# Kernel optimization log

Hardware: AMD Instinct MI355X
Metric: run time of the kernel (lower is better)

## Reference

```python
import jax, jax.numpy as jnp
import numpy as np
import math

DIM = 512


def setup_inputs() -> dict:
    key = jax.random.key(0)
    ks = jax.random.split(key, 6)
    B, N, D = 4, 4096, DIM
    H = D // 2
    features = jax.random.normal(ks[0], (B, N, D), dtype=jnp.float32)
    W1 = jax.random.normal(ks[1], (D, H), dtype=jnp.float32) * 0.02
    b1 = jnp.zeros((H,), dtype=jnp.float32)
    ln_g = jnp.ones((H,), dtype=jnp.float32)
    ln_b = jnp.zeros((H,), dtype=jnp.float32)
    W2 = jax.random.normal(ks[2], (H, 1), dtype=jnp.float32) * 0.02
    b2 = jnp.zeros((1,), dtype=jnp.float32)
    target_entropy = jnp.ones((1,), dtype=jnp.float32) * math.log(D)
    temperature = jnp.ones((1,), dtype=jnp.float32)
    return {"features": features, "W1": W1, "b1": b1, "ln_g": ln_g,
            "ln_b": ln_b, "W2": W2, "b2": b2,
            "target_entropy": target_entropy, "temperature": temperature}


def _layernorm(x, g, b, eps=1e-5):
    mu = jnp.mean(x, axis=-1, keepdims=True)
    var = jnp.mean((x - mu) ** 2, axis=-1, keepdims=True)
    return (x - mu) * jax.lax.rsqrt(var + eps) * g + b


def reference(features, W1, b1, ln_g, ln_b, W2, b2, target_entropy, temperature):
    # ---- compute_entropy: pairwise RBF kernel over [B, N, D] ----
    sq = jnp.sum(features ** 2, axis=-1)                       # [B, N]
    gram = jnp.einsum('bnd,bmd->bnm', features, features)      # [B, N, N]
    d2 = jnp.maximum(sq[:, :, None] + sq[:, None, :] - 2.0 * gram, 0.0)
    tau = temperature[0]
    kernel = jnp.exp(-d2 / (2.0 * tau ** 2))                   # [B, N, N]
    probs = kernel / jnp.sum(kernel, axis=-1, keepdims=True)
    entropy = -jnp.sum(probs * jnp.log(probs + 1e-6), axis=-1)  # [B, N]

    # ---- entropy estimator MLP (computed in original forward, output unused) ----
    h = features @ W1 + b1
    h = _layernorm(h, ln_g, ln_b)
    h = jax.nn.gelu(h, approximate=False)
    estimated_entropy = h @ W2 + b2                            # [B, N, 1] (unused)
    del estimated_entropy

    # ---- sigmoid-gated control signal ----
    entropy_diff = entropy - target_entropy[0]
    control_signal = jax.nn.sigmoid(-entropy_diff / tau)       # [B, N]
    controlled_features = features * control_signal[..., None]
    return controlled_features, control_signal
```

## Files before the change

### kernel.cpp

```cpp
#include <hip/hip_runtime.h>
#include <stdint.h>

#define N_TOK 4096
#define DIM   512
#define BATCH 4
#define BN    (BATCH * N_TOK)
#define JSPLIT 8
#define IPW   64
#define IPB   256
#define NG    (N_TOK / JSPLIT / 16)

typedef __attribute__((ext_vector_type(4))) float f32x4;
typedef __attribute__((ext_vector_type(8))) int   i32x8;

typedef const __attribute__((address_space(1))) uint32_t* gptr_t;
typedef __attribute__((address_space(3))) uint32_t* lptr_t;

__device__ __forceinline__ float sumsq8(uint lo, uint hi) {
    float s = 0.f, f;
    f = __builtin_amdgcn_cvt_f32_fp8((int)lo, 0); s = fmaf(f, f, s);
    f = __builtin_amdgcn_cvt_f32_fp8((int)lo, 1); s = fmaf(f, f, s);
    f = __builtin_amdgcn_cvt_f32_fp8((int)lo, 2); s = fmaf(f, f, s);
    f = __builtin_amdgcn_cvt_f32_fp8((int)lo, 3); s = fmaf(f, f, s);
    f = __builtin_amdgcn_cvt_f32_fp8((int)hi, 0); s = fmaf(f, f, s);
    f = __builtin_amdgcn_cvt_f32_fp8((int)hi, 1); s = fmaf(f, f, s);
    f = __builtin_amdgcn_cvt_f32_fp8((int)hi, 2); s = fmaf(f, f, s);
    f = __builtin_amdgcn_cvt_f32_fp8((int)hi, 3); s = fmaf(f, f, s);
    return s;
}

__global__ __launch_bounds__(256) void prep_kernel(
    const float* __restrict__ feat, uint8_t* __restrict__ fb,
    uint8_t* __restrict__ fbT, float* __restrict__ sq)
{
    __shared__ __align__(16) long lt[1024];
    const int t = threadIdx.x;
    const int row16 = t >> 4, seg = t & 15;
    const size_t grp = blockIdx.x;
    const size_t row = grp * 16 + row16;

    const float4* src = (const float4*)(feat + row * DIM + seg * 32);
    uint32_t wd[8];
    float s = 0.f;
#pragma unroll
    for (int i = 0; i < 4; ++i) {
        float4 a = src[2 * i], b = src[2 * i + 1];
        uint lo = (uint)__builtin_amdgcn_cvt_pk_fp8_f32(a.x, a.y, 0, false);
        lo      = (uint)__builtin_amdgcn_cvt_pk_fp8_f32(a.z, a.w, (int)lo, true);
        uint hi = (uint)__builtin_amdgcn_cvt_pk_fp8_f32(b.x, b.y, 0, false);
        hi      = (uint)__builtin_amdgcn_cvt_pk_fp8_f32(b.z, b.w, (int)hi, true);
        wd[2 * i] = lo; wd[2 * i + 1] = hi;
        s += sumsq8(lo, hi);
    }

    uint4* dst = (uint4*)(fb + row * DIM + seg * 32);
    uint4 o0; o0.x = wd[0]; o0.y = wd[1]; o0.z = wd[2]; o0.w = wd[3];
    uint4 o1; o1.x = wd[4]; o1.y = wd[5]; o1.z = wd[6]; o1.w = wd[7];
    dst[0] = o0; dst[1] = o1;

#pragma unroll
    for (int i = 0; i < 4; ++i) {
        int c = seg * 4 + i;
        long d = ((long)(unsigned)wd[2 * i + 1] << 32) | (unsigned)wd[2 * i];
        lt[c * 16 + ((row16 + c) & 15)] = d;
    }

#pragma unroll
    for (int m = 1; m < 16; m <<= 1) s += __shfl_xor(s, m);
    if (seg == 0) sq[row] = s;

    __syncthreads();
    long* ot = (long*)(fbT + grp * 8192);
#pragma unroll
    for (int i = 0; i < 4; ++i) {
        int p    = t + i * 256;
        int kk   = p >> 8;
        int rem  = p & 255;
        int half = rem >> 7;
        int l6   = (rem >> 1) & 63;
        int qq   = l6 >> 4;
        int r    = l6 & 15;
        int w8   = half * 2 + (p & 1);
        int c    = kk * 16 + qq * 4 + w8;
        ot[p] = lt[c * 16 + ((r + c) & 15)];
    }
}

__global__ __launch_bounds__(256, 2) void entropy_kernel(
    const uint8_t* __restrict__ fb, const uint8_t* __restrict__ fbT,
    const float* __restrict__ sq, const float* __restrict__ temp,
    float* __restrict__ Sp, float* __restrict__ Tp)
{
    __shared__ uint4 Bs[4][512];
    __shared__ float sqlds[NG * 16];
    const int t    = threadIdx.x;
    const int w    = t >> 6;
    const int lane = t & 63;
    const int q    = lane >> 4;
    const int c16  = lane & 15;
    const int lbo  = lane * 16;

    const int flat  = blockIdx.x;
    const int combo = flat & 31;
    const int batch = combo >> 3;
    const int jh    = combo & 7;
    const int iblk  = flat >> 5;
    const int iw    = iblk * IPB + w * IPW;
    const size_t rowbase = (size_t)batch * N_TOK;

    const float tau    = temp[0];
    const float inv2t2 = 0.5f / (tau * tau);
    const float cg     = 1.0f / (tau * tau);

    i32x8 afrag[4][4];
#pragma unroll
    for (int s = 0; s < 4; ++s) {
        const uint4* ap = (const uint4*)(fb + (rowbase + iw + s * 16 + c16) * DIM);
#pragma unroll
        for (int kk = 0; kk < 4; ++kk) {
            uint4 lo = ap[kk * 8 + q * 2];
            uint4 hi = ap[kk * 8 + q * 2 + 1];
            i32x8 v = {(int)lo.x, (int)lo.y, (int)lo.z, (int)lo.w,
                       (int)hi.x, (int)hi.y, (int)hi.z, (int)hi.w};
            afrag[s][kk] = v;
        }
    }
    float pi[4][4];
#pragma unroll
    for (int s = 0; s < 4; ++s)
#pragma unroll
        for (int r = 0; r < 4; ++r)
            pi[s][r] = -sq[rowbase + iw + s * 16 + q * 4 + r] * inv2t2;

    {
        const float* sqslice = sq + rowbase + (size_t)jh * (N_TOK / JSPLIT);
        sqlds[t]       = sqslice[t];
        sqlds[t + 256] = sqslice[t + 256];
    }

    float S[4][4], T[4][4];
#pragma unroll
    for (int s = 0; s < 4; ++s)
#pragma unroll
        for (int r = 0; r < 4; ++r) { S[s][r] = 0.f; T[s][r] = 0.f; }

    const uint8_t* bgbase = fbT
        + ((size_t)batch * (N_TOK / 16) + (size_t)jh * NG) * 8192;

    auto stage = [&](int g) {
        const uint8_t* gs = bgbase + (size_t)g * 8192 + w * 2048 + lbo;
        uint8_t* ld = (uint8_t*)(&Bs[g & 3][0]) + w * 2048;
        __builtin_amdgcn_global_load_lds((gptr_t)(const void*)gs,
                                         (lptr_t)(void*)ld, 16, 0, 0);
        __builtin_amdgcn_global_load_lds((gptr_t)(const void*)(gs + 1024),
                                         (lptr_t)(void*)(ld + 1024), 16, 0, 0);
    };
    stage(0);
    stage(1);
    asm volatile("s_waitcnt lgkmcnt(0)" ::: "memory");

    for (int g = 0; g < NG; ++g) {
        if (g + 2 < NG) stage(g + 2);
        if (g + 2 < NG)      asm volatile("s_waitcnt vmcnt(4)" ::: "memory");
        else if (g + 1 < NG) asm volatile("s_waitcnt vmcnt(2)" ::: "memory");
        else                 asm volatile("s_waitcnt vmcnt(0)" ::: "memory");
        __builtin_amdgcn_s_barrier();
        __builtin_amdgcn_sched_barrier(0);

        const uint8_t* bs = (const uint8_t*)(&Bs[g & 3][0]);
        float pj = -sqlds[g * 16 + c16] * inv2t2;
        f32x4 acc[4] = {{0,0,0,0},{0,0,0,0},{0,0,0,0},{0,0,0,0}};
        __builtin_amdgcn_s_setprio(1);
#pragma unroll
        for (int kk = 0; kk < 4; ++kk) {
            uint4 lo = *(const uint4*)(bs + kk * 2048 + lbo);
            uint4 hi = *(const uint4*)(bs + kk * 2048 + 1024 + lbo);
            i32x8 b = {(int)lo.x, (int)lo.y, (int)lo.z, (int)lo.w,
                       (int)hi.x, (int)hi.y, (int)hi.z, (int)hi.w};
            acc[0] = __builtin_amdgcn_mfma_scale_f32_16x16x128_f8f6f4(afrag[0][kk], b, acc[0], 0, 0, 0, 127, 0, 127);
            acc[1] = __builtin_amdgcn_mfma_scale_f32_16x16x128_f8f6f4(afrag[1][kk], b, acc[1], 0, 0, 0, 127, 0, 127);
            acc[2] = __builtin_amdgcn_mfma_scale_f32_16x16x128_f8f6f4(afrag[2][kk], b, acc[2], 0, 0, 0, 127, 0, 127);
            acc[3] = __builtin_amdgcn_mfma_scale_f32_16x16x128_f8f6f4(afrag[3][kk], b, acc[3], 0, 0, 0, 127, 0, 127);
        }
        __builtin_amdgcn_s_setprio(0);
        float m = -1e30f;
#pragma unroll
        for (int s = 0; s < 4; ++s)
#pragma unroll
            for (int r = 0; r < 4; ++r) {
                acc[s][r] = fmaf(acc[s][r], cg, pi[s][r] + pj);
                m = fmaxf(m, acc[s][r]);
            }
        if (m > -110.0f) {
#pragma unroll
            for (int s = 0; s < 4; ++s)
#pragma unroll
                for (int r = 0; r < 4; ++r) {
                    float ee = fminf(acc[s][r], 0.f);
                    float k  = __expf(ee);
                    S[s][r] += k;
                    T[s][r]  = fmaf(k, ee, T[s][r]);
                }
        }
    }

#pragma unroll
    for (int m = 1; m < 16; m <<= 1)
#pragma unroll
        for (int s = 0; s < 4; ++s)
#pragma unroll
            for (int r = 0; r < 4; ++r) {
                S[s][r] += __shfl_xor(S[s][r], m);
                T[s][r] += __shfl_xor(T[s][r], m);
            }

    if (c16 == 0) {
#pragma unroll
        for (int s = 0; s < 4; ++s)
#pragma unroll
            for (int r = 0; r < 4; ++r) {
                size_t idx = (size_t)jh * BN + rowbase + iw + s * 16 + q * 4 + r;
                Sp[idx] = S[s][r];
                Tp[idx] = T[s][r];
            }
    }
}

__global__ __launch_bounds__(256) void finalize_kernel(
    const float* __restrict__ feat, const float* __restrict__ Sp,
    const float* __restrict__ Tp, const float* __restrict__ tgt,
    const float* __restrict__ temp, float* __restrict__ out)
{
    int row  = (blockIdx.x << 2) + (threadIdx.x >> 6);
    int lane = threadIdx.x & 63;
    float S = 0.0f, T = 0.0f;
#pragma unroll
    for (int j = 0; j < JSPLIT; ++j) {
        S += Sp[(size_t)j * BN + row];
        T += Tp[(size_t)j * BN + row];
    }
    float tau = temp[0];
    float E  = __logf(S) - T / S;
    float cs = 1.0f / (1.0f + __expf((E - tgt[0]) / tau));

    const float4* F4 = (const float4*)(feat + (size_t)row * DIM);
    float4*       O4 = (float4*)(out + (size_t)row * DIM);
    float4 v0 = F4[lane], v1 = F4[lane + 64];
    v0.x *= cs; v0.y *= cs; v0.z *= cs; v0.w *= cs;
    v1.x *= cs; v1.y *= cs; v1.z *= cs; v1.w *= cs;
    O4[lane] = v0; O4[lane + 64] = v1;
    if (lane == 0) out[(size_t)BN * DIM + row] = cs;
}

extern "C" void kernel_launch(void* const* d_in, const int* in_sizes, int n_in,
                              void* d_out, int out_size, void* d_ws, size_t ws_size,
                              hipStream_t stream) {
    const float* feat = (const float*)d_in[0];
    const float* tgt  = (const float*)d_in[7];
    const float* temp = (const float*)d_in[8];
    float* out = (float*)d_out;

    char* ws = (char*)d_ws;
    uint8_t* fb  = (uint8_t*)ws;
    uint8_t* fbT = fb + (size_t)BN * DIM;
    float*   sq  = (float*)(fbT + (size_t)BN * DIM);
    float*   Sp  = sq + BN;
    float*   Tp  = Sp + (size_t)JSPLIT * BN;

    prep_kernel<<<dim3(BN / 16), dim3(256), 0, stream>>>(feat, fb, fbT, sq);
    entropy_kernel<<<dim3((N_TOK / IPB) * BATCH * JSPLIT), dim3(256), 0, stream>>>(fb, fbT, sq, temp, Sp, Tp);
    finalize_kernel<<<dim3(BN / 4), dim3(256), 0, stream>>>(feat, Sp, Tp, tgt, temp, out);
}
```

Baseline: 148.4 us.

## Use per-wave private LDS ring, drop row-major fp8 copy, bound-based exp skip

Each wave now stages the full B tile into its own double-buffered LDS slot. This removes the block-wide s_barrier from the inner loop; the next stage is issued after the MFMA reads complete. The row-major fp8 buffer is dropped and A fragments are loaded from the transposed fbT layout, which cuts prep writes. The skip test now uses an upper bound from the raw accumulator max and the max row norm, so the per-element FMA only runs when needed. Each wave now loads 4x more B data from global/L2 because tiles are no longer shared across the four waves, and LDS use doubles.

```diff
diff --git a/kernel.cpp b/kernel.cpp
--- a/kernel.cpp
+++ b/kernel.cpp
@@ -30,8 +30,8 @@
 }
 
 __global__ __launch_bounds__(256) void prep_kernel(
-    const float* __restrict__ feat, uint8_t* __restrict__ fb,
-    uint8_t* __restrict__ fbT, float* __restrict__ sq)
+    const float* __restrict__ feat, uint8_t* __restrict__ fbT,
+    float* __restrict__ sq)
 {
     __shared__ __align__(16) long lt[1024];
     const int t = threadIdx.x;
@@ -52,11 +52,6 @@
         wd[2 * i] = lo; wd[2 * i + 1] = hi;
         s += sumsq8(lo, hi);
     }
-
-    uint4* dst = (uint4*)(fb + row * DIM + seg * 32);
-    uint4 o0; o0.x = wd[0]; o0.y = wd[1]; o0.z = wd[2]; o0.w = wd[3];
-    uint4 o1; o1.x = wd[4]; o1.y = wd[5]; o1.z = wd[6]; o1.w = wd[7];
-    dst[0] = o0; dst[1] = o1;
 
 #pragma unroll
     for (int i = 0; i < 4; ++i) {
@@ -87,11 +82,11 @@
 }
 
 __global__ __launch_bounds__(256, 2) void entropy_kernel(
-    const uint8_t* __restrict__ fb, const uint8_t* __restrict__ fbT,
+    const uint8_t* __restrict__ fbT,
     const float* __restrict__ sq, const float* __restrict__ temp,
     float* __restrict__ Sp, float* __restrict__ Tp)
 {
-    __shared__ uint4 Bs[4][512];
+    __shared__ uint4 ring[4][2][512];
     __shared__ float sqlds[NG * 16];
     const int t    = threadIdx.x;
     const int w    = t >> 6;
@@ -110,28 +105,31 @@
 
     const float tau    = temp[0];
     const float inv2t2 = 0.5f / (tau * tau);
-    const float cg     = 1.0f / (tau * tau);
+    const float cg_    = 1.0f / (tau * tau);
 
     i32x8 afrag[4][4];
 #pragma unroll
     for (int s = 0; s < 4; ++s) {
-        const uint4* ap = (const uint4*)(fb + (rowbase + iw + s * 16 + c16) * DIM);
+        const uint8_t* ga = fbT + ((rowbase + iw) / 16 + s) * 8192;
 #pragma unroll
         for (int kk = 0; kk < 4; ++kk) {
-            uint4 lo = ap[kk * 8 + q * 2];
-            uint4 hi = ap[kk * 8 + q * 2 + 1];
+            uint4 lo = *(const uint4*)(ga + kk * 2048 + lbo);
+            uint4 hi = *(const uint4*)(ga + kk * 2048 + 1024 + lbo);
             i32x8 v = {(int)lo.x, (int)lo.y, (int)lo.z, (int)lo.w,
                        (int)hi.x, (int)hi.y, (int)hi.z, (int)hi.w};
             afrag[s][kk] = v;
         }
     }
-    float pi[4][4];
-#pragma unroll
-    for (int s = 0; s < 4; ++s)
-#pragma unroll
-        for (int r = 0; r < 4; ++r)
-            pi[s][r] = -sq[rowbase + iw + s * 16 + q * 4 + r] * inv2t2;
-
+    float pi_[4][4];
+    float pim = -1e30f;
+#pragma unroll
+    for (int s = 0; s < 4; ++s) {
+        float4 p4 = *(const float4*)(sq + rowbase + iw + s * 16 + q * 4);
+        pi_[s][0] = -p4.x * inv2t2; pi_[s][1] = -p4.y * inv2t2;
+        pi_[s][2] = -p4.z * inv2t2; pi_[s][3] = -p4.w * inv2t2;
+        pim = fmaxf(pim, fmaxf(fmaxf(pi_[s][0], pi_[s][1]),
+                               fmaxf(pi_[s][2], pi_[s][3])));
+    }
     {
         const float* sqslice = sq + rowbase + (size_t)jh * (N_TOK / JSPLIT);
         sqlds[t]       = sqslice[t];
@@ -147,56 +145,68 @@
     const uint8_t* bgbase = fbT
         + ((size_t)batch * (N_TOK / 16) + (size_t)jh * NG) * 8192;
 
-    auto stage = [&](int g) {
-        const uint8_t* gs = bgbase + (size_t)g * 8192 + w * 2048 + lbo;
-        uint8_t* ld = (uint8_t*)(&Bs[g & 3][0]) + w * 2048;
-        __builtin_amdgcn_global_load_lds((gptr_t)(const void*)gs,
-                                         (lptr_t)(void*)ld, 16, 0, 0);
-        __builtin_amdgcn_global_load_lds((gptr_t)(const void*)(gs + 1024),
-                                         (lptr_t)(void*)(ld + 1024), 16, 0, 0);
+    auto stage = [&](int g, int slot) {
+        const uint8_t* gs = bgbase + (size_t)g * 8192 + lbo;
+        uint8_t* ld = (uint8_t*)(&ring[w][slot][0]);
+#pragma unroll
+        for (int i = 0; i < 8; ++i)
+            __builtin_amdgcn_global_load_lds(
+                (gptr_t)(const void*)(gs + i * 1024),
+                (lptr_t)(void*)(ld + i * 1024), 16, 0, 0);
     };
-    stage(0);
-    stage(1);
+
+    stage(0, 0);
+    stage(1, 1);
     asm volatile("s_waitcnt lgkmcnt(0)" ::: "memory");
+    __builtin_amdgcn_s_barrier();
 
     for (int g = 0; g < NG; ++g) {
-        if (g + 2 < NG) stage(g + 2);
-        if (g + 2 < NG)      asm volatile("s_waitcnt vmcnt(4)" ::: "memory");
-        else if (g + 1 < NG) asm volatile("s_waitcnt vmcnt(2)" ::: "memory");
-        else                 asm volatile("s_waitcnt vmcnt(0)" ::: "memory");
-        __builtin_amdgcn_s_barrier();
+        if (g < NG - 1) asm volatile("s_waitcnt vmcnt(8)" ::: "memory");
+        else            asm volatile("s_waitcnt vmcnt(0)" ::: "memory");
         __builtin_amdgcn_sched_barrier(0);
 
-        const uint8_t* bs = (const uint8_t*)(&Bs[g & 3][0]);
+        const uint8_t* bs = (const uint8_t*)(&ring[w][g & 1][0]);
         float pj = -sqlds[g * 16 + c16] * inv2t2;
         f32x4 acc[4] = {{0,0,0,0},{0,0,0,0},{0,0,0,0},{0,0,0,0}};
         __builtin_amdgcn_s_setprio(1);
 #pragma unroll
-        for (int kk = 0; kk < 4; ++kk) {
-            uint4 lo = *(const uint4*)(bs + kk * 2048 + lbo);
-            uint4 hi = *(const uint4*)(bs + kk * 2048 + 1024 + lbo);
-            i32x8 b = {(int)lo.x, (int)lo.y, (int)lo.z, (int)lo.w,
-                       (int)hi.x, (int)hi.y, (int)hi.z, (int)hi.w};
-            acc[0] = __builtin_amdgcn_mfma_scale_f32_16x16x128_f8f6f4(afrag[0][kk], b, acc[0], 0, 0, 0, 127, 0, 127);
-            acc[1] = __builtin_amdgcn_mfma_scale_f32_16x16x128_f8f6f4(afrag[1][kk], b, acc[1], 0, 0, 0, 127, 0, 127);
-            acc[2] = __builtin_amdgcn_mfma_scale_f32_16x16x128_f8f6f4(afrag[2][kk], b, acc[2], 0, 0, 0, 127, 0, 127);
-            acc[3] = __builtin_amdgcn_mfma_scale_f32_16x16x128_f8f6f4(afrag[3][kk], b, acc[3], 0, 0, 0, 127, 0, 127);
+        for (int kk = 0; kk < 4; kk += 2) {
+            uint4 l0 = *(const uint4*)(bs + kk * 2048 + lbo);
+            uint4 h0 = *(const uint4*)(bs + kk * 2048 + 1024 + lbo);
+            uint4 l1 = *(const uint4*)(bs + (kk + 1) * 2048 + lbo);
+            uint4 h1 = *(const uint4*)(bs + (kk + 1) * 2048 + 1024 + lbo);
+            i32x8 b0 = {(int)l0.x, (int)l0.y, (int)l0.z, (int)l0.w,
+                        (int)h0.x, (int)h0.y, (int)h0.z, (int)h0.w};
+            i32x8 b1 = {(int)l1.x, (int)l1.y, (int)l1.z, (int)l1.w,
+                        (int)h1.x, (int)h1.y, (int)h1.z, (int)h1.w};
+            acc[0] = __builtin_amdgcn_mfma_scale_f32_16x16x128_f8f6f4(afrag[0][kk], b0, acc[0], 0, 0, 0, 127, 0, 127);
+            acc[1] = __builtin_amdgcn_mfma_scale_f32_16x16x128_f8f6f4(afrag[1][kk], b0, acc[1], 0, 0, 0, 127, 0, 127);
+            acc[2] = __builtin_amdgcn_mfma_scale_f32_16x16x128_f8f6f4(afrag[2][kk], b0, acc[2], 0, 0, 0, 127, 0, 127);
+            acc[3] = __builtin_amdgcn_mfma_scale_f32_16x16x128_f8f6f4(afrag[3][kk], b0, acc[3], 0, 0, 0, 127, 0, 127);
+            acc[0] = __builtin_amdgcn_mfma_scale_f32_16x16x128_f8f6f4(afrag[0][kk+1], b1, acc[0], 0, 0, 0, 127, 0, 127);
+            acc[1] = __builtin_amdgcn_mfma_scale_f32_16x16x128_f8f6f4(afrag[1][kk+1], b1, acc[1], 0, 0, 0, 127, 0, 127);
+            acc[2] = __builtin_amdgcn_mfma_scale_f32_16x16x128_f8f6f4(afrag[2][kk+1], b1, acc[2], 0, 0, 0, 127, 0, 127);
+            acc[3] = __builtin_amdgcn_mfma_scale_f32_16x16x128_f8f6f4(afrag[3][kk+1], b1, acc[3], 0, 0, 0, 127, 0, 127);
         }
         __builtin_amdgcn_s_setprio(0);
-        float m = -1e30f;
-#pragma unroll
-        for (int s = 0; s < 4; ++s)
-#pragma unroll
-            for (int r = 0; r < 4; ++r) {
-                acc[s][r] = fmaf(acc[s][r], cg, pi[s][r] + pj);
-                m = fmaxf(m, acc[s][r]);
-            }
-        if (m > -110.0f) {
+
+        asm volatile("s_waitcnt lgkmcnt(0)" ::: "memory");
+        __builtin_amdgcn_sched_barrier(0);
+        if (g + 2 < NG) stage(g + 2, g & 1);
+
+        float m0 = fmaxf(fmaxf(acc[0][0], acc[0][1]), fmaxf(acc[0][2], acc[0][3]));
+        float m1 = fmaxf(fmaxf(acc[1][0], acc[1][1]), fmaxf(acc[1][2], acc[1][3]));
+        float m2 = fmaxf(fmaxf(acc[2][0], acc[2][1]), fmaxf(acc[2][2], acc[2][3]));
+        float m3 = fmaxf(fmaxf(acc[3][0], acc[3][1]), fmaxf(acc[3][2], acc[3][3]));
+        float mm = fmaxf(fmaxf(m0, m1), fmaxf(m2, m3));
+        float bound = fmaf(mm, cg_, pim + pj);
+        if (bound > -110.0f) {
 #pragma unroll
             for (int s = 0; s < 4; ++s)
 #pragma unroll
                 for (int r = 0; r < 4; ++r) {
-                    float ee = fminf(acc[s][r], 0.f);
+                    float e  = fmaf(acc[s][r], cg_, pi_[s][r] + pj);
+                    float ee = fminf(e, 0.f);
                     float k  = __expf(ee);
                     S[s][r] += k;
                     T[s][r]  = fmaf(k, ee, T[s][r]);
@@ -261,13 +271,12 @@
     float* out = (float*)d_out;
 
     char* ws = (char*)d_ws;
-    uint8_t* fb  = (uint8_t*)ws;
-    uint8_t* fbT = fb + (size_t)BN * DIM;
+    uint8_t* fbT = (uint8_t*)ws;
     float*   sq  = (float*)(fbT + (size_t)BN * DIM);
     float*   Sp  = sq + BN;
     float*   Tp  = Sp + (size_t)JSPLIT * BN;
 
-    prep_kernel<<<dim3(BN / 16), dim3(256), 0, stream>>>(feat, fb, fbT, sq);
-    entropy_kernel<<<dim3((N_TOK / IPB) * BATCH * JSPLIT), dim3(256), 0, stream>>>(fb, fbT, sq, temp, Sp, Tp);
+    prep_kernel<<<dim3(BN / 16), dim3(256), 0, stream>>>(feat, fbT, sq);
+    entropy_kernel<<<dim3((N_TOK / IPB) * BATCH * JSPLIT), dim3(256), 0, stream>>>(fbT, sq, temp, Sp, Tp);
     finalize_kernel<<<dim3(BN / 4), dim3(256), 0, stream>>>(feat, Sp, Tp, tgt, temp, out);
 }
```

Measured after the change: 145.2 us. 1.02x faster.
